# Kernel optimization log

Hardware: AMD Instinct MI355X
Metric: run time of the kernel (lower is better)

The kernel has to match this reference:

```python
import jax, jax.numpy as jnp
import numpy as np

N_NODES = 50000
N_EDGES = 800000
D = 128  # in_dim == hidden_dim


def setup_inputs() -> dict:
    key = jax.random.key(0)
    k1, k2, k3, k4 = jax.random.split(key, 4)
    x = jax.random.normal(k1, (N_NODES, D), dtype=jnp.float32)
    edge_index = jax.random.randint(k2, (2, N_EDGES), 0, N_NODES, dtype=jnp.int64)
    # Glorot-ish scale for square weights
    scale = 1.0 / np.sqrt(D)
    W1 = jax.random.normal(k3, (D, D), dtype=jnp.float32) * scale
    W2 = jax.random.normal(k4, (D, D), dtype=jnp.float32) * scale
    b1 = jnp.zeros((D,), dtype=jnp.float32)
    b2 = jnp.zeros((D,), dtype=jnp.float32)
    return {"x": x, "edge_index": edge_index, "W1": W1, "b1": b1, "W2": W2, "b2": b2}


def _gcn_layer(x, W, b, src, dst, norm, n):
    # PyG GCNConv: h = x @ W, then symmetric-normalized scatter-add, then + bias
    h = x @ W                                   # [N, D] dense GEMM
    msg = h[src] * norm[:, None]                # [E', D] gather + scale
    out = jax.ops.segment_sum(msg, dst, num_segments=n)  # scatter-add
    return out + b


def reference(x, edge_index, W1, b1, W2, b2):
    n = x.shape[0]
    # add self-loops (GCNConv default add_self_loops=True)
    loops = jnp.arange(n, dtype=edge_index.dtype)
    src = jnp.concatenate([edge_index[0], loops])
    dst = jnp.concatenate([edge_index[1], loops])
    # symmetric normalization: deg^{-1/2}[src] * deg^{-1/2}[dst]
    deg = jax.ops.segment_sum(jnp.ones_like(src, dtype=x.dtype), dst, num_segments=n)
    dinv = jax.lax.rsqrt(jnp.maximum(deg, 1.0))  # deg >= 1 due to self-loops
    norm = dinv[src] * dinv[dst]
    # layer 1: conv -> relu (dropout is identity in eval mode)
    h = jax.nn.relu(_gcn_layer(x, W1, b1, src, dst, norm, n))
    # layer 2 (cut='c2'): conv -> relu
    h = jax.nn.relu(_gcn_layer(h, W2, b2, src, dst, norm, n))
    return h
```

## Files before the change

### kernel.cpp

```cpp
#include <hip/hip_runtime.h>

#define NN 50000
#define NE 800000
#define DD 128
#define NSTRIP 3125
#define NB 196
#define CHUNK 4096
#define MAXB 6144

#define OF_BCNT  0
#define OF_BBASE 256
#define OF_BCUR  768
#define OF_DINV  1024
#define OF_OFFS  51200
#define OF_TMP   101632
#define OF_CSRU  901632
#define OF_G     1301632
#define OF_X2    4501632
#define OF_W1H   10901632
#define OF_W1L   10909824
#define OF_W2H   10918016
#define OF_W2L   10926208

typedef __attribute__((ext_vector_type(8))) short bf8_t;
typedef __attribute__((ext_vector_type(4))) float f32x4;

static __device__ __forceinline__ unsigned short f2bf(float f) {
    unsigned int u = __float_as_uint(f);
    unsigned int r = (u + 0x7fffu + ((u >> 16) & 1u)) >> 16;
    return (unsigned short)r;
}
static __device__ __forceinline__ float bf2f(unsigned short h) {
    return __uint_as_float(((unsigned int)h) << 16);
}

__global__ void k_zero(int* __restrict__ bcnt) {
    bcnt[threadIdx.x] = 0;
}

__global__ void k_hist(const int* __restrict__ dst, int* __restrict__ bcnt) {
    __shared__ int lc[256];
    int tid = threadIdx.x;
    lc[tid] = 0;
    __syncthreads();
    int e0 = blockIdx.x * CHUNK;
    int e1 = e0 + CHUNK; if (e1 > NE) e1 = NE;
    for (int e = e0 + tid; e < e1; e += 256)
        atomicAdd(&lc[dst[e] >> 8], 1);
    __syncthreads();
    if (lc[tid]) atomicAdd(&bcnt[tid], lc[tid]);
}

__global__ void k_bscan(const int* __restrict__ bcnt, int* __restrict__ bbase,
                        int* __restrict__ bcur, int* __restrict__ offs) {
    __shared__ int sh[256];
    int tid = threadIdx.x;
    int v = bcnt[tid];
    sh[tid] = v;
    __syncthreads();
    for (int o = 1; o < 256; o <<= 1) {
        int t = (tid >= o) ? sh[tid - o] : 0;
        __syncthreads();
        sh[tid] += t;
        __syncthreads();
    }
    bbase[tid] = sh[tid] - v;
    bcur[tid]  = sh[tid] - v;
    if (tid == 255) bbase[256] = sh[255];
    if (tid == 0) offs[NN] = NE;
}

__global__ void k_shuf(const int* __restrict__ src, const int* __restrict__ dst,
                       int* __restrict__ bcur, unsigned int* __restrict__ tmp) {
    __shared__ int lcnt[256];
    __shared__ int lbase[256];
    __shared__ int lcur[256];
    int tid = threadIdx.x;
    lcnt[tid] = 0;
    __syncthreads();
    int e0 = blockIdx.x * CHUNK;
    int e1 = e0 + CHUNK; if (e1 > NE) e1 = NE;
    for (int e = e0 + tid; e < e1; e += 256)
        atomicAdd(&lcnt[dst[e] >> 8], 1);
    __syncthreads();
    if (lcnt[tid]) lbase[tid] = atomicAdd(&bcur[tid], lcnt[tid]);
    lcur[tid] = 0;
    __syncthreads();
    for (int e = e0 + tid; e < e1; e += 256) {
        int d = dst[e], s = src[e];
        int b = d >> 8;
        int r = atomicAdd(&lcur[b], 1);
        tmp[lbase[b] + r] = ((unsigned int)s << 8) | (unsigned int)(d & 255);
    }
}

__global__ __launch_bounds__(256) void k_sort(const int* __restrict__ bbase,
                                              const unsigned int* __restrict__ tmp,
                                              ushort* __restrict__ csru,
                                              int* __restrict__ offs,
                                              float* __restrict__ dinv) {
    __shared__ unsigned int ent[MAXB];
    __shared__ int cnt[256];
    __shared__ int boff[256];
    __shared__ int cur[256];
    int b = blockIdx.x, tid = threadIdx.x;
    int base = bbase[b];
    int nb = bbase[b + 1] - base;
    cnt[tid] = 0;
    __syncthreads();
    for (int i = tid; i < nb; i += 256) {
        unsigned int v = tmp[base + i];
        ent[i] = v;
        atomicAdd(&cnt[v & 255], 1);
    }
    __syncthreads();
    int v = cnt[tid];
    boff[tid] = v;
    __syncthreads();
    for (int o = 1; o < 256; o <<= 1) {
        int t = (tid >= o) ? boff[tid - o] : 0;
        __syncthreads();
        boff[tid] += t;
        __syncthreads();
    }
    int excl = boff[tid] - v;
    int node = b * 256 + tid;
    if (node < NN) {
        offs[node] = base + excl;
        dinv[node] = rsqrtf((float)(v + 1));
    }
    cur[tid] = excl;
    __syncthreads();
    for (int i = tid; i < nb; i += 256) {
        unsigned int e = ent[i];
        int bin = e & 255;
        int r = atomicAdd(&cur[bin], 1);
        csru[base + r] = (ushort)(e >> 8);
    }
}

__global__ void k_wconv(const float* __restrict__ W, ushort* __restrict__ wh,
                        ushort* __restrict__ wl) {
    int g = blockIdx.x * blockDim.x + threadIdx.x;
    if (g >= 2048) return;
    int ntile = g >> 8;
    int kk = (g >> 6) & 3;
    int lane = g & 63;
    int k0 = kk * 32 + ((lane >> 4) * 8);
    int col = ntile * 16 + (lane & 15);
#pragma unroll
    for (int j = 0; j < 8; ++j) {
        float w = W[(k0 + j) * DD + col];
        unsigned short h = f2bf(w);
        wh[(size_t)g * 8 + j] = h;
        wl[(size_t)g * 8 + j] = f2bf(w - bf2f(h));
    }
}

__global__ __launch_bounds__(256) void k_mgemm(const float* __restrict__ X,
                                               const ushort* __restrict__ wh,
                                               const ushort* __restrict__ wl,
                                               const float* __restrict__ dinv,
                                               ushort* __restrict__ G) {
    int wave = threadIdx.x >> 6;
    int lane = threadIdx.x & 63;
    int strip = blockIdx.x * 4 + wave;
    if (strip >= NSTRIP) return;
    int rb = strip << 4;
    int m = lane & 15;
    int quad = lane >> 4;
    const float* ar = X + (size_t)(rb + m) * DD;
    f32x4 acc[8];
#pragma unroll
    for (int t = 0; t < 8; ++t) acc[t] = (f32x4){0.f, 0.f, 0.f, 0.f};
#pragma unroll
    for (int kk = 0; kk < 4; ++kk) {
        float4 xa = *(const float4*)(ar + kk * 32 + quad * 8);
        float4 xb = *(const float4*)(ar + kk * 32 + quad * 8 + 4);
        float xs[8] = {xa.x, xa.y, xa.z, xa.w, xb.x, xb.y, xb.z, xb.w};
        bf8_t ah, al;
#pragma unroll
        for (int j = 0; j < 8; ++j) {
            unsigned short hh = f2bf(xs[j]);
            ah[j] = (short)hh;
            al[j] = (short)f2bf(xs[j] - bf2f(hh));
        }
#pragma unroll
        for (int t = 0; t < 8; ++t) {
            size_t bo = ((size_t)(t * 4 + kk) * 64 + lane) * 8;
            bf8_t bh = *(const bf8_t*)(wh + bo);
            bf8_t bl = *(const bf8_t*)(wl + bo);
            acc[t] = __builtin_amdgcn_mfma_f32_16x16x32_bf16(ah, bh, acc[t], 0, 0, 0);
            acc[t] = __builtin_amdgcn_mfma_f32_16x16x32_bf16(ah, bl, acc[t], 0, 0, 0);
            acc[t] = __builtin_amdgcn_mfma_f32_16x16x32_bf16(al, bh, acc[t], 0, 0, 0);
        }
    }
    float dv[4];
#pragma unroll
    for (int r = 0; r < 4; ++r) dv[r] = dinv[rb + quad * 4 + r];
#pragma unroll
    for (int t = 0; t < 8; ++t) {
#pragma unroll
        for (int r = 0; r < 4; ++r)
            G[(size_t)(rb + quad * 4 + r) * DD + t * 16 + m] = f2bf(dv[r] * acc[t][r]);
    }
}

__global__ void k_agg(const ushort* __restrict__ g, const float* __restrict__ dinv,
                      const int* __restrict__ offs, const ushort* __restrict__ csru,
                      const float* __restrict__ bias, float* __restrict__ outf) {
    int gid = blockIdx.x * blockDim.x + threadIdx.x;
    int node = gid >> 6;
    if (node >= NN) return;
    int lane = threadIdx.x & 63;
    int half = lane >> 5;
    int c = lane & 31;
    float4 a0 = {0.f, 0.f, 0.f, 0.f};
    float4 a1 = {0.f, 0.f, 0.f, 0.f};
    int e  = offs[node] + half;
    int e1 = offs[node + 1];
    for (; e + 2 < e1; e += 4) {
        int s0 = csru[e];
        int s1 = csru[e + 2];
        ushort4 v0 = *(const ushort4*)(g + (size_t)s0 * DD + 4 * c);
        ushort4 v1 = *(const ushort4*)(g + (size_t)s1 * DD + 4 * c);
        a0.x += bf2f(v0.x); a0.y += bf2f(v0.y); a0.z += bf2f(v0.z); a0.w += bf2f(v0.w);
        a1.x += bf2f(v1.x); a1.y += bf2f(v1.y); a1.z += bf2f(v1.z); a1.w += bf2f(v1.w);
    }
    if (e < e1) {
        int s0 = csru[e];
        ushort4 v0 = *(const ushort4*)(g + (size_t)s0 * DD + 4 * c);
        a0.x += bf2f(v0.x); a0.y += bf2f(v0.y); a0.z += bf2f(v0.z); a0.w += bf2f(v0.w);
    }
    if (half == 0) {
        ushort4 v = *(const ushort4*)(g + (size_t)node * DD + 4 * c);
        a0.x += bf2f(v.x); a0.y += bf2f(v.y); a0.z += bf2f(v.z); a0.w += bf2f(v.w);
    }
    a0.x += a1.x; a0.y += a1.y; a0.z += a1.z; a0.w += a1.w;
    a0.x += __shfl_xor(a0.x, 32, 64);
    a0.y += __shfl_xor(a0.y, 32, 64);
    a0.z += __shfl_xor(a0.z, 32, 64);
    a0.w += __shfl_xor(a0.w, 32, 64);
    if (half == 0) {
        float di = dinv[node];
        float4 bv = ((const float4*)bias)[c];
        float4 o;
        o.x = fmaxf(di * a0.x + bv.x, 0.f);
        o.y = fmaxf(di * a0.y + bv.y, 0.f);
        o.z = fmaxf(di * a0.z + bv.z, 0.f);
        o.w = fmaxf(di * a0.w + bv.w, 0.f);
        ((float4*)(outf + (size_t)node * DD))[c] = o;
    }
}

extern "C" void kernel_launch(void* const* d_in, const int* in_sizes, int n_in,
                              void* d_out, int out_size, void* d_ws, size_t ws_size,
                              hipStream_t stream) {
    const float* x  = (const float*)d_in[0];
    const int*   ei = (const int*)d_in[1];
    const float* W1 = (const float*)d_in[2];
    const float* b1 = (const float*)d_in[3];
    const float* W2 = (const float*)d_in[4];
    const float* b2 = (const float*)d_in[5];
    float* out = (float*)d_out;

    const int* src = ei;
    const int* dst = ei + NE;

    int*          wsi  = (int*)d_ws;
    float*        wsf  = (float*)d_ws;
    ushort*       wsu  = (ushort*)d_ws;
    unsigned int* wsuw = (unsigned int*)d_ws;
    int*    bcnt  = wsi + OF_BCNT;
    int*    bbase = wsi + OF_BBASE;
    int*    bcur  = wsi + OF_BCUR;
    float*  dinv  = wsf + OF_DINV;
    int*    offs  = wsi + OF_OFFS;
    unsigned int* tmp = wsuw + OF_TMP;
    ushort* csru  = wsu + (size_t)OF_CSRU * 2;
    ushort* gbuf  = wsu + (size_t)OF_G * 2;
    float*  x2    = wsf + OF_X2;
    ushort* w1h   = wsu + (size_t)OF_W1H * 2;
    ushort* w1l   = wsu + (size_t)OF_W1L * 2;
    ushort* w2h   = wsu + (size_t)OF_W2H * 2;
    ushort* w2l   = wsu + (size_t)OF_W2L * 2;

    const int chunks = (NE + CHUNK - 1) / CHUNK;

    hipLaunchKernelGGL(k_zero,  dim3(1), dim3(256), 0, stream, bcnt);
    hipLaunchKernelGGL(k_hist,  dim3(chunks), dim3(256), 0, stream, dst, bcnt);
    hipLaunchKernelGGL(k_bscan, dim3(1), dim3(256), 0, stream, bcnt, bbase, bcur, offs);
    hipLaunchKernelGGL(k_shuf,  dim3(chunks), dim3(256), 0, stream, src, dst, bcur, tmp);
    hipLaunchKernelGGL(k_sort,  dim3(NB), dim3(256), 0, stream, bbase, tmp, csru, offs, dinv);

    hipLaunchKernelGGL(k_wconv, dim3(8), dim3(256), 0, stream, W1, w1h, w1l);
    hipLaunchKernelGGL(k_wconv, dim3(8), dim3(256), 0, stream, W2, w2h, w2l);

    const int gblocks = (NSTRIP + 3) / 4;

    hipLaunchKernelGGL(k_mgemm, dim3(gblocks), dim3(256), 0, stream, x, w1h, w1l, dinv, gbuf);
    hipLaunchKernelGGL(k_agg,   dim3((NN * 64 + 255) / 256), dim3(256), 0, stream,
                       gbuf, dinv, offs, csru, b1, x2);
    hipLaunchKernelGGL(k_mgemm, dim3(gblocks), dim3(256), 0, stream, x2, w2h, w2l, dinv, gbuf);
    hipLaunchKernelGGL(k_agg,   dim3((NN * 64 + 255) / 256), dim3(256), 0, stream,
                       gbuf, dinv, offs, csru, b2, out);
}
```

Measured before the change: 232.2 us.

## Tile feature buffer into 32-column slabs and aggregate per slab for cache locality

The GEMM now writes the bf16 intermediate as four column slabs of 32 features each, laid out [tile][node][32]. Aggregation runs one pass per slab, with blocks ordered by slab so a 3.2MB slab stays resident in cache during the random gathers. Each wave now handles a single node's 32 columns with four edges in flight. The two weight-conversion launches and the zeroing kernel are merged into one launch. The cost is more aggregation blocks, re-reading the CSR indices four times, and narrower 4-byte gathers.

```diff
diff --git a/kernel.cpp b/kernel.cpp
--- a/kernel.cpp
+++ b/kernel.cpp
@@ -7,6 +7,7 @@
 #define NB 196
 #define CHUNK 4096
 #define MAXB 6144
+#define BPT 12500
 
 #define OF_BCNT  0
 #define OF_BBASE 256
@@ -34,8 +35,28 @@
     return __uint_as_float(((unsigned int)h) << 16);
 }
 
-__global__ void k_zero(int* __restrict__ bcnt) {
-    bcnt[threadIdx.x] = 0;
+__global__ void k_wconv(const float* __restrict__ W1, const float* __restrict__ W2,
+                        ushort* __restrict__ w1h, ushort* __restrict__ w1l,
+                        ushort* __restrict__ w2h, ushort* __restrict__ w2l,
+                        int* __restrict__ bcnt) {
+    if (blockIdx.x == 0) bcnt[threadIdx.x] = 0;
+    int gg = blockIdx.x * 256 + threadIdx.x;
+    const float* W = (gg < 2048) ? W1 : W2;
+    ushort* wh = (gg < 2048) ? w1h : w2h;
+    ushort* wl = (gg < 2048) ? w1l : w2l;
+    int g = gg & 2047;
+    int ntile = g >> 8;
+    int kk = (g >> 6) & 3;
+    int lane = g & 63;
+    int k0 = kk * 32 + ((lane >> 4) * 8);
+    int col = ntile * 16 + (lane & 15);
+#pragma unroll
+    for (int j = 0; j < 8; ++j) {
+        float w = W[(k0 + j) * DD + col];
+        unsigned short h = f2bf(w);
+        wh[(size_t)g * 8 + j] = h;
+        wl[(size_t)g * 8 + j] = f2bf(w - bf2f(h));
+    }
 }
 
 __global__ void k_hist(const int* __restrict__ dst, int* __restrict__ bcnt) {
@@ -136,24 +157,6 @@
         int bin = e & 255;
         int r = atomicAdd(&cur[bin], 1);
         csru[base + r] = (ushort)(e >> 8);
-    }
-}
-
-__global__ void k_wconv(const float* __restrict__ W, ushort* __restrict__ wh,
-                        ushort* __restrict__ wl) {
-    int g = blockIdx.x * blockDim.x + threadIdx.x;
-    if (g >= 2048) return;
-    int ntile = g >> 8;
-    int kk = (g >> 6) & 3;
-    int lane = g & 63;
-    int k0 = kk * 32 + ((lane >> 4) * 8);
-    int col = ntile * 16 + (lane & 15);
-#pragma unroll
-    for (int j = 0; j < 8; ++j) {
-        float w = W[(k0 + j) * DD + col];
-        unsigned short h = f2bf(w);
-        wh[(size_t)g * 8 + j] = h;
-        wl[(size_t)g * 8 + j] = f2bf(w - bf2f(h));
     }
 }
 
@@ -200,56 +203,57 @@
     for (int r = 0; r < 4; ++r) dv[r] = dinv[rb + quad * 4 + r];
 #pragma unroll
     for (int t = 0; t < 8; ++t) {
+        int tile = t >> 1;
+        int cin  = (t & 1) * 16 + m;
 #pragma unroll
         for (int r = 0; r < 4; ++r)
-            G[(size_t)(rb + quad * 4 + r) * DD + t * 16 + m] = f2bf(dv[r] * acc[t][r]);
+            G[((size_t)tile * NN + (rb + quad * 4 + r)) * 32 + cin] =
+                f2bf(dv[r] * acc[t][r]);
     }
 }
 
 __global__ void k_agg(const ushort* __restrict__ g, const float* __restrict__ dinv,
                       const int* __restrict__ offs, const ushort* __restrict__ csru,
                       const float* __restrict__ bias, float* __restrict__ outf) {
-    int gid = blockIdx.x * blockDim.x + threadIdx.x;
-    int node = gid >> 6;
-    if (node >= NN) return;
+    int wave = threadIdx.x >> 6;
     int lane = threadIdx.x & 63;
-    int half = lane >> 5;
-    int c = lane & 31;
-    float4 a0 = {0.f, 0.f, 0.f, 0.f};
-    float4 a1 = {0.f, 0.f, 0.f, 0.f};
-    int e  = offs[node] + half;
+    int tile = blockIdx.x / BPT;
+    int node = (blockIdx.x % BPT) * 4 + wave;
+    int q = lane >> 4;
+    int l = lane & 15;
+    const ushort* gt = g + (size_t)tile * NN * 32;
+    float2 a0 = {0.f, 0.f}, a1 = {0.f, 0.f};
+    int e  = offs[node] + q;
     int e1 = offs[node + 1];
-    for (; e + 2 < e1; e += 4) {
+    for (; e + 4 < e1; e += 8) {
         int s0 = csru[e];
-        int s1 = csru[e + 2];
-        ushort4 v0 = *(const ushort4*)(g + (size_t)s0 * DD + 4 * c);
-        ushort4 v1 = *(const ushort4*)(g + (size_t)s1 * DD + 4 * c);
-        a0.x += bf2f(v0.x); a0.y += bf2f(v0.y); a0.z += bf2f(v0.z); a0.w += bf2f(v0.w);
-        a1.x += bf2f(v1.x); a1.y += bf2f(v1.y); a1.z += bf2f(v1.z); a1.w += bf2f(v1.w);
+        int s1 = csru[e + 4];
+        ushort2 v0 = *(const ushort2*)(gt + (size_t)s0 * 32 + 2 * l);
+        ushort2 v1 = *(const ushort2*)(gt + (size_t)s1 * 32 + 2 * l);
+        a0.x += bf2f(v0.x); a0.y += bf2f(v0.y);
+        a1.x += bf2f(v1.x); a1.y += bf2f(v1.y);
     }
     if (e < e1) {
         int s0 = csru[e];
-        ushort4 v0 = *(const ushort4*)(g + (size_t)s0 * DD + 4 * c);
-        a0.x += bf2f(v0.x); a0.y += bf2f(v0.y); a0.z += bf2f(v0.z); a0.w += bf2f(v0.w);
-    }
-    if (half == 0) {
-        ushort4 v = *(const ushort4*)(g + (size_t)node * DD + 4 * c);
-        a0.x += bf2f(v.x); a0.y += bf2f(v.y); a0.z += bf2f(v.z); a0.w += bf2f(v.w);
-    }
-    a0.x += a1.x; a0.y += a1.y; a0.z += a1.z; a0.w += a1.w;
+        ushort2 v0 = *(const ushort2*)(gt + (size_t)s0 * 32 + 2 * l);
+        a0.x += bf2f(v0.x); a0.y += bf2f(v0.y);
+    }
+    if (q == 0) {
+        ushort2 v = *(const ushort2*)(gt + (size_t)node * 32 + 2 * l);
+        a0.x += bf2f(v.x); a0.y += bf2f(v.y);
+    }
+    a0.x += a1.x; a0.y += a1.y;
+    a0.x += __shfl_xor(a0.x, 16, 64);
+    a0.y += __shfl_xor(a0.y, 16, 64);
     a0.x += __shfl_xor(a0.x, 32, 64);
     a0.y += __shfl_xor(a0.y, 32, 64);
-    a0.z += __shfl_xor(a0.z, 32, 64);
-    a0.w += __shfl_xor(a0.w, 32, 64);
-    if (half == 0) {
+    if (q == 0) {
         float di = dinv[node];
-        float4 bv = ((const float4*)bias)[c];
-        float4 o;
+        float2 bv = *(const float2*)(bias + tile * 32 + 2 * l);
+        float2 o;
         o.x = fmaxf(di * a0.x + bv.x, 0.f);
         o.y = fmaxf(di * a0.y + bv.y, 0.f);
-        o.z = fmaxf(di * a0.z + bv.z, 0.f);
-        o.w = fmaxf(di * a0.w + bv.w, 0.f);
-        ((float4*)(outf + (size_t)node * DD))[c] = o;
+        *(float2*)(outf + (size_t)node * DD + tile * 32 + 2 * l) = o;
     }
 }
 
@@ -287,21 +291,19 @@
 
     const int chunks = (NE + CHUNK - 1) / CHUNK;
 
-    hipLaunchKernelGGL(k_zero,  dim3(1), dim3(256), 0, stream, bcnt);
+    hipLaunchKernelGGL(k_wconv, dim3(16), dim3(256), 0, stream,
+                       W1, W2, w1h, w1l, w2h, w2l, bcnt);
     hipLaunchKernelGGL(k_hist,  dim3(chunks), dim3(256), 0, stream, dst, bcnt);
     hipLaunchKernelGGL(k_bscan, dim3(1), dim3(256), 0, stream, bcnt, bbase, bcur, offs);
     hipLaunchKernelGGL(k_shuf,  dim3(chunks), dim3(256), 0, stream, src, dst, bcur, tmp);
     hipLaunchKernelGGL(k_sort,  dim3(NB), dim3(256), 0, stream, bbase, tmp, csru, offs, dinv);
 
-    hipLaunchKernelGGL(k_wconv, dim3(8), dim3(256), 0, stream, W1, w1h, w1l);
-    hipLaunchKernelGGL(k_wconv, dim3(8), dim3(256), 0, stream, W2, w2h, w2l);
-
     const int gblocks = (NSTRIP + 3) / 4;
 
     hipLaunchKernelGGL(k_mgemm, dim3(gblocks), dim3(256), 0, stream, x, w1h, w1l, dinv, gbuf);
-    hipLaunchKernelGGL(k_agg,   dim3((NN * 64 + 255) / 256), dim3(256), 0, stream,
+    hipLaunchKernelGGL(k_agg,   dim3(4 * BPT), dim3(256), 0, stream,
                        gbuf, dinv, offs, csru, b1, x2);
     hipLaunchKernelGGL(k_mgemm, dim3(gblocks), dim3(256), 0, stream, x2, w2h, w2l, dinv, gbuf);
-    hipLaunchKernelGGL(k_agg,   dim3((NN * 64 + 255) / 256), dim3(256), 0, stream,
+    hipLaunchKernelGGL(k_agg,   dim3(4 * BPT), dim3(256), 0, stream,
                        gbuf, dinv, offs, csru, b2, out);
 }
```

Result: slower. 314.4 us (+35.4%).
